# Optimization experiments

Hardware: AMD Instinct MI355X
Metric: run time of the kernel (lower is better)

The kernel has to match this reference:

```python
import jax, jax.numpy as jnp
import numpy as np

CODEBOOK_SIZE = 1024
CODEBOOK_DIM = 64
COMMITMENT_WEIGHT = 0.25
DECAY = 0.99
EPS = 1e-5


def setup_inputs() -> dict:
    key = jax.random.key(0)
    k1, k2, k3 = jax.random.split(key, 3)
    B, D, T = 32, CODEBOOK_DIM, 4096
    z = jax.random.normal(k1, (B, D, T), dtype=jnp.float32)
    embedding = jax.random.normal(k2, (CODEBOOK_SIZE, CODEBOOK_DIM), dtype=jnp.float32)
    cluster_size = jnp.zeros((CODEBOOK_SIZE,), dtype=jnp.float32)
    embed_avg = jax.random.normal(k3, (CODEBOOK_SIZE, CODEBOOK_DIM), dtype=jnp.float32)
    return {"z": z, "embedding": embedding, "cluster_size": cluster_size, "embed_avg": embed_avg}


def reference(z, embedding, cluster_size, embed_avg):
    # z: [B, D, T]; embedding/embed_avg: [K, D]; cluster_size: [K]
    B, D, T = z.shape
    K = embedding.shape[0]
    z_flat = jnp.transpose(z, (0, 2, 1)).reshape(-1, D)  # [N, D], N = B*T

    # squared-euclidean distances via expansion (matches torch cdist expansion)
    dist = (
        jnp.sum(z_flat * z_flat, axis=1, keepdims=True)
        + jnp.sum(embedding * embedding, axis=1)
        - 2.0 * (z_flat @ embedding.T)
    )  # [N, K]
    indices = jnp.argmin(dist, axis=1)  # [N] int

    # EMA updates (training path). one_hot.sum(0) -> segment count; one_hot.T @ z_flat -> segment sum
    counts = jax.ops.segment_sum(jnp.ones(z_flat.shape[0], dtype=z_flat.dtype), indices, num_segments=K)
    new_cluster_size = cluster_size * DECAY + (1.0 - DECAY) * counts
    embed_sum = jax.ops.segment_sum(z_flat, indices, num_segments=K)  # [K, D]
    new_embed_avg = embed_avg * DECAY + (1.0 - DECAY) * embed_sum
    n = jnp.sum(new_cluster_size)
    smoothed = (new_cluster_size + EPS) / (n + K * EPS) * n  # Laplace smoothing
    new_embedding = new_embed_avg / smoothed[:, None]  # [K, D]

    # quantize with the *updated* codebook (as in the torch in-place update)
    z_q_flat = new_embedding[indices]  # [N, D] gather
    loss = COMMITMENT_WEIGHT * jnp.mean((z_flat - jax.lax.stop_gradient(z_q_flat)) ** 2)
    # straight-through estimator
    z_q_flat = z_flat + jax.lax.stop_gradient(z_q_flat - z_flat)
    z_q = jnp.transpose(z_q_flat.reshape(B, T, D), (0, 2, 1))  # [B, D, T]
    return z_q, loss, indices.reshape(B, T)
```

## Files before the change

### kernel.cpp

```cpp
#include <hip/hip_runtime.h>

#define N_PTS 131072
#define TD 4096
#define DD 64
#define KK 1024
#define MARGIN_TH 2e-3f

typedef short bf16x8 __attribute__((ext_vector_type(8)));
typedef float f32x4  __attribute__((ext_vector_type(4)));

__device__ inline unsigned short f2bf(float f) {
    unsigned u = __float_as_uint(f);
    unsigned r = u + 0x7FFFu + ((u >> 16) & 1u);
    return (unsigned short)(r >> 16);
}
__device__ inline float bf2f(unsigned short h) {
    return __uint_as_float(((unsigned)h) << 16);
}

__global__ __launch_bounds__(256) void vq_prep(const float* __restrict__ z,
                                               unsigned short* __restrict__ zh,
                                               unsigned short* __restrict__ zl)
{
    __shared__ float tile[64][65];
    const int tid = threadIdx.x;
    const int b = blockIdx.x >> 6;
    const int t0 = (blockIdx.x & 63) * 64;

    const int d = tid >> 2, tq = tid & 3;
#pragma unroll
    for (int it = 0; it < 4; ++it) {
        const int tt = tq * 16 + it * 4;
        const float4 v = *(const float4*)(z + ((size_t)b * DD + d) * TD + t0 + tt);
        tile[d][tt] = v.x; tile[d][tt + 1] = v.y; tile[d][tt + 2] = v.z; tile[d][tt + 3] = v.w;
    }
    __syncthreads();

    const int p = tid >> 2, dg = tid & 3;
    bf16x8 h0, h1, l0, l1;
#pragma unroll
    for (int j = 0; j < 8; ++j) {
        const float v0 = -tile[dg * 16 + j][p];
        const unsigned short a = f2bf(v0);
        h0[j] = (short)a; l0[j] = (short)f2bf(v0 - bf2f(a));
        const float v1 = -tile[dg * 16 + 8 + j][p];
        const unsigned short c = f2bf(v1);
        h1[j] = (short)c; l1[j] = (short)f2bf(v1 - bf2f(c));
    }
    const size_t o = ((size_t)(b * TD + t0 + p)) * DD + dg * 16;
    *(bf16x8*)(zh + o) = h0;
    *(bf16x8*)(zh + o + 8) = h1;
    *(bf16x8*)(zl + o) = l0;
    *(bf16x8*)(zl + o + 8) = l1;
}

__global__ __launch_bounds__(256) void vq_eprep(const float* __restrict__ emb,
                                                unsigned short* __restrict__ efh,
                                                unsigned short* __restrict__ efl,
                                                float* __restrict__ halfnorm)
{
    const int k = blockIdx.x * 256 + threadIdx.x;
    if (k >= KK) return;
    const int t = k >> 4, col = k & 15;
    const float* e = emb + (size_t)k * DD;
    double s = 0.0;
#pragma unroll
    for (int d = 0; d < DD; ++d) {
        const float v = e[d];
        const double dv = (double)v;
        s = fma(dv, dv, s);
        const unsigned short h = f2bf(v);
        const int q = d >> 3, j = d & 7;
        const size_t pos = (size_t)t * 1024 + (q >> 2) * 512 + ((q & 3) * 16 + col) * 8 + j;
        efh[pos] = h;
        efl[pos] = f2bf(v - bf2f(h));
    }
    halfnorm[k] = (float)(0.5 * s);
}

__global__ __launch_bounds__(256, 4) void vq_screen_mfma(
    const unsigned short* __restrict__ zh, const unsigned short* __restrict__ zl,
    const unsigned short* __restrict__ efh, const unsigned short* __restrict__ efl,
    const float* __restrict__ hn,
    int* __restrict__ idx_ws, float* __restrict__ ind_out,
    int* __restrict__ nflag, int* __restrict__ flags, int* __restrict__ hist)
{
    const int tid  = threadIdx.x;
    const int lane = tid & 63;
    const int wv   = tid >> 6;
    const int quad = lane >> 4;
    const int col  = lane & 15;
    const int pbase = blockIdx.x * 128 + wv * 32;

    const bf16x8* pA0h = (const bf16x8*)(zh + (size_t)(pbase + col) * DD + quad * 8);
    const bf16x8* pA0l = (const bf16x8*)(zl + (size_t)(pbase + col) * DD + quad * 8);
    const bf16x8* pA1h = (const bf16x8*)(zh + (size_t)(pbase + 16 + col) * DD + quad * 8);
    const bf16x8* pA1l = (const bf16x8*)(zl + (size_t)(pbase + 16 + col) * DD + quad * 8);
    const bf16x8 A0h0 = pA0h[0], A0h1 = pA0h[4];
    const bf16x8 A0l0 = pA0l[0], A0l1 = pA0l[4];
    const bf16x8 A1h0 = pA1h[0], A1h1 = pA1h[4];
    const bf16x8 A1l0 = pA1l[0], A1l1 = pA1l[4];

    const unsigned short* fh = efh + lane * 8;
    const unsigned short* fl = efl + lane * 8;

    bf16x8 ch0 = *(const bf16x8*)(fh);
    bf16x8 ch1 = *(const bf16x8*)(fh + 512);
    bf16x8 cl0 = *(const bf16x8*)(fl);
    bf16x8 cl1 = *(const bf16x8*)(fl + 512);
    float chn = hn[col];

    float best0[4]  = {1e30f, 1e30f, 1e30f, 1e30f};
    float best20[4] = {1e30f, 1e30f, 1e30f, 1e30f};
    int   bidx0[4]  = {0, 0, 0, 0};
    float best1[4]  = {1e30f, 1e30f, 1e30f, 1e30f};
    float best21[4] = {1e30f, 1e30f, 1e30f, 1e30f};
    int   bidx1[4]  = {0, 0, 0, 0};

#pragma unroll 2
    for (int t = 0; t < KK / 16; ++t) {
        const int tn = (t + 1) & 63;
        const bf16x8 nh0 = *(const bf16x8*)(fh + tn * 1024);
        const bf16x8 nh1 = *(const bf16x8*)(fh + tn * 1024 + 512);
        const bf16x8 nl0 = *(const bf16x8*)(fl + tn * 1024);
        const bf16x8 nl1 = *(const bf16x8*)(fl + tn * 1024 + 512);
        const float  nhn = hn[tn * 16 + col];

        f32x4 a0 = {chn, chn, chn, chn};
        f32x4 a1 = {chn, chn, chn, chn};
        a0 = __builtin_amdgcn_mfma_f32_16x16x32_bf16(A0h0, ch0, a0, 0, 0, 0);
        a1 = __builtin_amdgcn_mfma_f32_16x16x32_bf16(A1h0, ch0, a1, 0, 0, 0);
        a0 = __builtin_amdgcn_mfma_f32_16x16x32_bf16(A0h1, ch1, a0, 0, 0, 0);
        a1 = __builtin_amdgcn_mfma_f32_16x16x32_bf16(A1h1, ch1, a1, 0, 0, 0);
        a0 = __builtin_amdgcn_mfma_f32_16x16x32_bf16(A0l0, ch0, a0, 0, 0, 0);
        a1 = __builtin_amdgcn_mfma_f32_16x16x32_bf16(A1l0, ch0, a1, 0, 0, 0);
        a0 = __builtin_amdgcn_mfma_f32_16x16x32_bf16(A0l1, ch1, a0, 0, 0, 0);
        a1 = __builtin_amdgcn_mfma_f32_16x16x32_bf16(A1l1, ch1, a1, 0, 0, 0);
        a0 = __builtin_amdgcn_mfma_f32_16x16x32_bf16(A0h0, cl0, a0, 0, 0, 0);
        a1 = __builtin_amdgcn_mfma_f32_16x16x32_bf16(A1h0, cl0, a1, 0, 0, 0);
        a0 = __builtin_amdgcn_mfma_f32_16x16x32_bf16(A0h1, cl1, a0, 0, 0, 0);
        a1 = __builtin_amdgcn_mfma_f32_16x16x32_bf16(A1h1, cl1, a1, 0, 0, 0);

        const int code = t * 16 + col;
#pragma unroll
        for (int r = 0; r < 4; ++r) {
            const float s0 = a0[r];
            best20[r] = __builtin_amdgcn_fmed3f(best0[r], best20[r], s0);
            if (s0 < best0[r]) { best0[r] = s0; bidx0[r] = code; }
            const float s1 = a1[r];
            best21[r] = __builtin_amdgcn_fmed3f(best1[r], best21[r], s1);
            if (s1 < best1[r]) { best1[r] = s1; bidx1[r] = code; }
        }

        ch0 = nh0; ch1 = nh1; cl0 = nl0; cl1 = nl1; chn = nhn;
    }

#pragma unroll
    for (int off = 1; off < 16; off <<= 1) {
#pragma unroll
        for (int r = 0; r < 4; ++r) {
            {
                const float ob  = __shfl_xor(best0[r],  off, 64);
                const float ob2 = __shfl_xor(best20[r], off, 64);
                const int   oi  = __shfl_xor(bidx0[r],  off, 64);
                const float nb2 = fminf(fminf(best20[r], ob2), fmaxf(best0[r], ob));
                if (ob < best0[r]) { best0[r] = ob; bidx0[r] = oi; }
                best20[r] = nb2;
            }
            {
                const float ob  = __shfl_xor(best1[r],  off, 64);
                const float ob2 = __shfl_xor(best21[r], off, 64);
                const int   oi  = __shfl_xor(bidx1[r],  off, 64);
                const float nb2 = fminf(fminf(best21[r], ob2), fmaxf(best1[r], ob));
                if (ob < best1[r]) { best1[r] = ob; bidx1[r] = oi; }
                best21[r] = nb2;
            }
        }
    }

    if (col == 0) {
#pragma unroll
        for (int r = 0; r < 4; ++r) {
            const int n0 = pbase + quad * 4 + r;
            idx_ws[n0] = bidx0[r];
            ind_out[n0] = (float)bidx0[r];
            atomicAdd(&hist[bidx0[r]], 1);
            if (best20[r] - best0[r] < MARGIN_TH) {
                const int pos = atomicAdd(nflag, 1);
                flags[pos] = n0;
            }
            const int n1 = pbase + 16 + quad * 4 + r;
            idx_ws[n1] = bidx1[r];
            ind_out[n1] = (float)bidx1[r];
            atomicAdd(&hist[bidx1[r]], 1);
            if (best21[r] - best1[r] < MARGIN_TH) {
                const int pos = atomicAdd(nflag, 1);
                flags[pos] = n1;
            }
        }
    }
}

__global__ __launch_bounds__(256) void vq_fallback(
    const float* __restrict__ z, const float* __restrict__ emb,
    int* __restrict__ idx_ws, float* __restrict__ ind_out,
    const int* __restrict__ nflag, const int* __restrict__ flags,
    int* __restrict__ hist)
{
    __shared__ float zs[4][DD];
    const int total = *nflag;
    const int lane = threadIdx.x & 63;
    const int wid = threadIdx.x >> 6;
    const int gw = blockIdx.x * 4 + wid;

    for (int i = gw; i < total; i += gridDim.x * 4) {
        const int n = flags[i];
        const int b = n >> 12, t = n & 4095;
        zs[wid][lane] = z[((size_t)b * DD + lane) * TD + t];
        __builtin_amdgcn_s_waitcnt(0);
        double best = 1e300;
        int bi = KK;
        for (int kc = 0; kc < KK / 64; ++kc) {
            const int k = kc * 64 + lane;
            const float4* e = (const float4*)(emb + (size_t)k * DD);
            double dot = 0.0, nn = 0.0;
#pragma unroll
            for (int j = 0; j < 16; ++j) {
                float4 ev = e[j];
                double e0 = (double)ev.x, e1 = (double)ev.y, e2 = (double)ev.z, e3 = (double)ev.w;
                nn = fma(e0, e0, fma(e1, e1, fma(e2, e2, fma(e3, e3, nn))));
                dot = fma((double)zs[wid][4 * j + 0], e0,
                      fma((double)zs[wid][4 * j + 1], e1,
                      fma((double)zs[wid][4 * j + 2], e2,
                      fma((double)zs[wid][4 * j + 3], e3, dot))));
            }
            double s = 0.5 * nn - dot;
            if (s < best || (s == best && k < bi)) { best = s; bi = k; }
        }
        for (int off = 32; off > 0; off >>= 1) {
            double os = __shfl_down(best, off, 64);
            int oi = __shfl_down(bi, off, 64);
            if (os < best || (os == best && oi < bi)) { best = os; bi = oi; }
        }
        if (lane == 0) {
            const int old = idx_ws[n];
            if (bi != old) {
                idx_ws[n] = bi;
                ind_out[n] = (float)bi;
                atomicAdd(&hist[old], -1);
                atomicAdd(&hist[bi], 1);
            }
        }
    }
}

__global__ __launch_bounds__(1024) void vq_prefix_smo(
    const int* __restrict__ hist, const float* __restrict__ cs,
    int* __restrict__ cursor, float* __restrict__ rsmo)
{
    __shared__ int tmp[KK];
    __shared__ double dred[KK];
    const int k = threadIdx.x;
    const int c = hist[k];
    tmp[k] = c;
    const double ncs = 0.99 * (double)cs[k] + 0.01 * (double)c;
    dred[k] = ncs;
    __syncthreads();
    for (int off = 1; off < KK; off <<= 1) {
        int u = (k >= off) ? tmp[k - off] : 0;
        __syncthreads();
        tmp[k] += u;
        __syncthreads();
    }
    cursor[k] = tmp[k] - c;
    for (int s = 512; s > 0; s >>= 1) {
        if (k < s) dred[k] += dred[k + s];
        __syncthreads();
    }
    const double nsum = dred[0];
    const double smo = (ncs + 1e-5) / (nsum + (double)KK * 1e-5) * nsum;
    rsmo[k] = (float)(1.0 / smo);
}

__global__ __launch_bounds__(256) void vq_scatter(const int* __restrict__ idx_ws,
                                                  int* __restrict__ cursor, int* __restrict__ order)
{
    const int n = blockIdx.x * 256 + threadIdx.x;
    const int bi = idx_ws[n];
    const int pos = atomicAdd(&cursor[bi], 1);
    order[pos] = n;
}

__global__ __launch_bounds__(256) void vq_esum2(
    const unsigned short* __restrict__ zh, const unsigned short* __restrict__ zl,
    const int* __restrict__ idx_ws, const int* __restrict__ order,
    float* __restrict__ esum)
{
    const int tid = threadIdx.x;
    const int lane = tid & 63;
    const int w = tid >> 6;
    const int base = blockIdx.x * 256 + w * 64;

    const int pid_l = order[base + lane];
    const int code_l = idx_ws[pid_l];

    float v[64];
#pragma unroll
    for (int j = 0; j < 64; ++j) {
        const int pj = __shfl(pid_l, j, 64);
        const size_t o = (size_t)pj * DD + lane;
        v[j] = bf2f(zh[o]) + bf2f(zl[o]);
    }

    float racc = 0.f;
    int cur = __shfl(code_l, 0, 64);
#pragma unroll
    for (int j = 0; j < 64; ++j) {
        const int cj = __shfl(code_l, j, 64);
        if (cj != cur) {
            atomicAdd(&esum[(size_t)cur * DD + lane], -racc);
            racc = 0.f;
            cur = cj;
        }
        racc += v[j];
    }
    atomicAdd(&esum[(size_t)cur * DD + lane], -racc);
}

__global__ __launch_bounds__(256) void vq_newE(
    const float* __restrict__ avg, const float* __restrict__ esum,
    const float* __restrict__ rsmo, float* __restrict__ newE)
{
    const int j = blockIdx.x * 256 + threadIdx.x;
    newE[j] = (float)((0.99 * (double)avg[j] + 0.01 * (double)esum[j]) * (double)rsmo[j >> 6]);
}

__global__ __launch_bounds__(256) void vq_gather_loss(
    const float* __restrict__ z, const float* __restrict__ newE,
    const int* __restrict__ idx_ws, float* __restrict__ zq_out,
    double* __restrict__ loss_acc, int* __restrict__ done_cnt,
    float* __restrict__ loss_out)
{
    const int tid = threadIdx.x;
    const int n = blockIdx.x * 256 + tid;
    const int b = n >> 12;
    const int t = n & 4095;
    const float* zb = z + ((size_t)b * DD) * TD + t;
    float* ob = zq_out + ((size_t)b * DD) * TD + t;
    const int bi = idx_ws[n];
    const float* e = newE + (size_t)bi * DD;
    double acc = 0.0;
#pragma unroll
    for (int d = 0; d < DD; ++d) {
        float q = e[d];
        float zv = zb[(size_t)d * TD];
        ob[(size_t)d * TD] = q;
        float df = zv - q;
        acc = fma((double)df, (double)df, acc);
    }
    for (int off = 32; off > 0; off >>= 1) acc += __shfl_down(acc, off, 64);
    __shared__ double wsum[4];
    const int wid = tid >> 6, lane = tid & 63;
    if (lane == 0) wsum[wid] = acc;
    __syncthreads();
    if (tid == 0) {
        atomicAdd(loss_acc, wsum[0] + wsum[1] + wsum[2] + wsum[3]);
        __threadfence();
        const int prev = atomicAdd(done_cnt, 1);
        if (prev == gridDim.x - 1) {
            __threadfence();
            *loss_out = (float)(0.25 * (*loss_acc) / (double)(N_PTS * DD));
        }
    }
}

extern "C" void kernel_launch(void* const* d_in, const int* in_sizes, int n_in,
                              void* d_out, int out_size, void* d_ws, size_t ws_size,
                              hipStream_t stream) {
    const float* z    = (const float*)d_in[0];
    const float* emb  = (const float*)d_in[1];
    const float* cs   = (const float*)d_in[2];
    const float* avg  = (const float*)d_in[3];

    float* out      = (float*)d_out;
    float* zq_out   = out;
    float* loss_out = out + 8388608;
    float* ind_out  = out + 8388609;

    unsigned short* zh = (unsigned short*)d_out;
    unsigned short* zl = (unsigned short*)((char*)d_out + 16777216);

    char* ws = (char*)d_ws;
    int*            idx_ws   = (int*)ws;
    float*          newE     = (float*)(ws + 524288);
    float*          esum     = (float*)(ws + 786432);
    int*            hist     = (int*)(ws + 1048576);
    int*            nflag    = (int*)(ws + 1052672);
    int*            done_cnt = (int*)(ws + 1052676);
    double*         loss_acc = (double*)(ws + 1052680);
    float*          halfnorm = (float*)(ws + 1052688);
    int*            cursor   = (int*)(ws + 1056784);
    int*            flags    = (int*)(ws + 1060880);
    int*            order    = (int*)(ws + 1585168);
    unsigned short* efh      = (unsigned short*)(ws + 2109456);
    unsigned short* efl      = (unsigned short*)(ws + 2240528);
    float*          rsmo     = (float*)(ws + 2371600);

    hipMemsetAsync(ws + 786432, 0, 266256, stream);

    vq_prep<<<2048, 256, 0, stream>>>(z, zh, zl);
    vq_eprep<<<4, 256, 0, stream>>>(emb, efh, efl, halfnorm);
    vq_screen_mfma<<<1024, 256, 0, stream>>>(zh, zl, efh, efl, halfnorm,
                                             idx_ws, ind_out, nflag, flags, hist);
    vq_fallback<<<128, 256, 0, stream>>>(z, emb, idx_ws, ind_out, nflag, flags, hist);
    vq_prefix_smo<<<1, 1024, 0, stream>>>(hist, cs, cursor, rsmo);
    vq_scatter<<<N_PTS / 256, 256, 0, stream>>>(idx_ws, cursor, order);
    vq_esum2<<<N_PTS / 256, 256, 0, stream>>>(zh, zl, idx_ws, order, esum);
    vq_newE<<<256, 256, 0, stream>>>(avg, esum, rsmo, newE);
    vq_gather_loss<<<N_PTS / 256, 256, 0, stream>>>(z, newE, idx_ws, zq_out,
                                                    loss_acc, done_cnt, loss_out);
}
```

Measured before the change: 342.0 us.

## Stage codebook tiles through LDS with async global-to-LDS loads and triple buffering

```diff
diff --git a/kernel.cpp b/kernel.cpp
--- a/kernel.cpp
+++ b/kernel.cpp
@@ -16,6 +16,12 @@
 }
 __device__ inline float bf2f(unsigned short h) {
     return __uint_as_float(((unsigned)h) << 16);
+}
+
+__device__ inline void gload_lds16(const unsigned short* g, unsigned short* l) {
+    __builtin_amdgcn_global_load_lds(
+        (const __attribute__((address_space(1))) unsigned int*)g,
+        (__attribute__((address_space(3))) unsigned int*)l, 16, 0, 0);
 }
 
 __global__ __launch_bounds__(256) void vq_prep(const float* __restrict__ z,
@@ -85,11 +91,15 @@
     int* __restrict__ idx_ws, float* __restrict__ ind_out,
     int* __restrict__ nflag, int* __restrict__ flags, int* __restrict__ hist)
 {
+    __shared__ __align__(16) unsigned short tiles[4][2048];
+    __shared__ float hns[KK];
+
     const int tid  = threadIdx.x;
     const int lane = tid & 63;
     const int wv   = tid >> 6;
     const int quad = lane >> 4;
     const int col  = lane & 15;
+    const int loff = lane * 8;
     const int pbase = blockIdx.x * 128 + wv * 32;
 
     const bf16x8* pA0h = (const bf16x8*)(zh + (size_t)(pbase + col) * DD + quad * 8);
@@ -101,14 +111,18 @@
     const bf16x8 A1h0 = pA1h[0], A1h1 = pA1h[4];
     const bf16x8 A1l0 = pA1l[0], A1l1 = pA1l[4];
 
-    const unsigned short* fh = efh + lane * 8;
-    const unsigned short* fl = efl + lane * 8;
-
-    bf16x8 ch0 = *(const bf16x8*)(fh);
-    bf16x8 ch1 = *(const bf16x8*)(fh + 512);
-    bf16x8 cl0 = *(const bf16x8*)(fl);
-    bf16x8 cl1 = *(const bf16x8*)(fl + 512);
-    float chn = hn[col];
+    ((float4*)hns)[tid] = ((const float4*)hn)[tid];
+
+    const unsigned short* sgl = (wv < 2 ? efh : efl) + (tid & 127) * 8;
+
+    asm volatile("s_waitcnt vmcnt(0)" ::: "memory");
+    __builtin_amdgcn_sched_barrier(0);
+    __syncthreads();
+
+#define SCREEN_STAGE(T) gload_lds16(sgl + (size_t)(T) * 1024, &tiles[(T) & 3][tid * 8])
+
+    SCREEN_STAGE(0);
+    SCREEN_STAGE(1);
 
     float best0[4]  = {1e30f, 1e30f, 1e30f, 1e30f};
     float best20[4] = {1e30f, 1e30f, 1e30f, 1e30f};
@@ -117,43 +131,61 @@
     float best21[4] = {1e30f, 1e30f, 1e30f, 1e30f};
     int   bidx1[4]  = {0, 0, 0, 0};
 
-#pragma unroll 2
-    for (int t = 0; t < KK / 16; ++t) {
-        const int tn = (t + 1) & 63;
-        const bf16x8 nh0 = *(const bf16x8*)(fh + tn * 1024);
-        const bf16x8 nh1 = *(const bf16x8*)(fh + tn * 1024 + 512);
-        const bf16x8 nl0 = *(const bf16x8*)(fl + tn * 1024);
-        const bf16x8 nl1 = *(const bf16x8*)(fl + tn * 1024 + 512);
-        const float  nhn = hn[tn * 16 + col];
-
-        f32x4 a0 = {chn, chn, chn, chn};
-        f32x4 a1 = {chn, chn, chn, chn};
-        a0 = __builtin_amdgcn_mfma_f32_16x16x32_bf16(A0h0, ch0, a0, 0, 0, 0);
-        a1 = __builtin_amdgcn_mfma_f32_16x16x32_bf16(A1h0, ch0, a1, 0, 0, 0);
-        a0 = __builtin_amdgcn_mfma_f32_16x16x32_bf16(A0h1, ch1, a0, 0, 0, 0);
-        a1 = __builtin_amdgcn_mfma_f32_16x16x32_bf16(A1h1, ch1, a1, 0, 0, 0);
-        a0 = __builtin_amdgcn_mfma_f32_16x16x32_bf16(A0l0, ch0, a0, 0, 0, 0);
-        a1 = __builtin_amdgcn_mfma_f32_16x16x32_bf16(A1l0, ch0, a1, 0, 0, 0);
-        a0 = __builtin_amdgcn_mfma_f32_16x16x32_bf16(A0l1, ch1, a0, 0, 0, 0);
-        a1 = __builtin_amdgcn_mfma_f32_16x16x32_bf16(A1l1, ch1, a1, 0, 0, 0);
-        a0 = __builtin_amdgcn_mfma_f32_16x16x32_bf16(A0h0, cl0, a0, 0, 0, 0);
-        a1 = __builtin_amdgcn_mfma_f32_16x16x32_bf16(A1h0, cl0, a1, 0, 0, 0);
-        a0 = __builtin_amdgcn_mfma_f32_16x16x32_bf16(A0h1, cl1, a0, 0, 0, 0);
-        a1 = __builtin_amdgcn_mfma_f32_16x16x32_bf16(A1h1, cl1, a1, 0, 0, 0);
-
-        const int code = t * 16 + col;
-#pragma unroll
-        for (int r = 0; r < 4; ++r) {
-            const float s0 = a0[r];
-            best20[r] = __builtin_amdgcn_fmed3f(best0[r], best20[r], s0);
-            if (s0 < best0[r]) { best0[r] = s0; bidx0[r] = code; }
-            const float s1 = a1[r];
-            best21[r] = __builtin_amdgcn_fmed3f(best1[r], best21[r], s1);
-            if (s1 < best1[r]) { best1[r] = s1; bidx1[r] = code; }
-        }
-
-        ch0 = nh0; ch1 = nh1; cl0 = nl0; cl1 = nl1; chn = nhn;
-    }
+#define SCREEN_BODY(T)                                                              \
+    {                                                                               \
+        const unsigned short* buf = &tiles[(T) & 3][0];                             \
+        const bf16x8 Bh0 = *(const bf16x8*)(buf + loff);                            \
+        const bf16x8 Bh1 = *(const bf16x8*)(buf + 512 + loff);                      \
+        const bf16x8 Bl0 = *(const bf16x8*)(buf + 1024 + loff);                     \
+        const bf16x8 Bl1 = *(const bf16x8*)(buf + 1536 + loff);                     \
+        const float chn = hns[(T) * 16 + col];                                      \
+        f32x4 a0 = {chn, chn, chn, chn};                                            \
+        f32x4 a1 = {chn, chn, chn, chn};                                            \
+        a0 = __builtin_amdgcn_mfma_f32_16x16x32_bf16(A0h0, Bh0, a0, 0, 0, 0);       \
+        a1 = __builtin_amdgcn_mfma_f32_16x16x32_bf16(A1h0, Bh0, a1, 0, 0, 0);       \
+        a0 = __builtin_amdgcn_mfma_f32_16x16x32_bf16(A0h1, Bh1, a0, 0, 0, 0);       \
+        a1 = __builtin_amdgcn_mfma_f32_16x16x32_bf16(A1h1, Bh1, a1, 0, 0, 0);       \
+        a0 = __builtin_amdgcn_mfma_f32_16x16x32_bf16(A0l0, Bh0, a0, 0, 0, 0);       \
+        a1 = __builtin_amdgcn_mfma_f32_16x16x32_bf16(A1l0, Bh0, a1, 0, 0, 0);       \
+        a0 = __builtin_amdgcn_mfma_f32_16x16x32_bf16(A0l1, Bh1, a0, 0, 0, 0);       \
+        a1 = __builtin_amdgcn_mfma_f32_16x16x32_bf16(A1l1, Bh1, a1, 0, 0, 0);       \
+        a0 = __builtin_amdgcn_mfma_f32_16x16x32_bf16(A0h0, Bl0, a0, 0, 0, 0);       \
+        a1 = __builtin_amdgcn_mfma_f32_16x16x32_bf16(A1h0, Bl0, a1, 0, 0, 0);       \
+        a0 = __builtin_amdgcn_mfma_f32_16x16x32_bf16(A0h1, Bl1, a0, 0, 0, 0);       \
+        a1 = __builtin_amdgcn_mfma_f32_16x16x32_bf16(A1h1, Bl1, a1, 0, 0, 0);       \
+        const int code = (T) * 16 + col;                                            \
+        _Pragma("unroll")                                                           \
+        for (int r = 0; r < 4; ++r) {                                               \
+            const float s0 = a0[r];                                                 \
+            best20[r] = __builtin_amdgcn_fmed3f(best0[r], best20[r], s0);           \
+            if (s0 < best0[r]) { best0[r] = s0; bidx0[r] = code; }                  \
+            const float s1 = a1[r];                                                 \
+            best21[r] = __builtin_amdgcn_fmed3f(best1[r], best21[r], s1);           \
+            if (s1 < best1[r]) { best1[r] = s1; bidx1[r] = code; }                  \
+        }                                                                           \
+    }
+
+    for (int t = 0; t < 62; ++t) {
+        SCREEN_STAGE(t + 2);
+        asm volatile("s_waitcnt vmcnt(2)" ::: "memory");
+        __builtin_amdgcn_sched_barrier(0);
+        __builtin_amdgcn_s_barrier();
+        __builtin_amdgcn_sched_barrier(0);
+        SCREEN_BODY(t);
+    }
+    asm volatile("s_waitcnt vmcnt(1)" ::: "memory");
+    __builtin_amdgcn_sched_barrier(0);
+    __builtin_amdgcn_s_barrier();
+    __builtin_amdgcn_sched_barrier(0);
+    SCREEN_BODY(62);
+    asm volatile("s_waitcnt vmcnt(0)" ::: "memory");
+    __builtin_amdgcn_sched_barrier(0);
+    __builtin_amdgcn_s_barrier();
+    __builtin_amdgcn_sched_barrier(0);
+    SCREEN_BODY(63);
+
+#undef SCREEN_STAGE
+#undef SCREEN_BODY
 
 #pragma unroll
     for (int off = 1; off < 16; off <<= 1) {
```

After: 342.6 us. Within noise of the previous version (+0.2%).

## Stage codebook tiles in LDS via direct global-to-LDS loads in screen kernel

Applied to the files above, without the earlier changes.

```diff
diff --git a/kernel.cpp b/kernel.cpp
--- a/kernel.cpp
+++ b/kernel.cpp
@@ -16,6 +16,12 @@
 }
 __device__ inline float bf2f(unsigned short h) {
     return __uint_as_float(((unsigned)h) << 16);
+}
+
+__device__ inline void gload_lds16(const unsigned short* g, unsigned short* l) {
+    __builtin_amdgcn_global_load_lds(
+        (const __attribute__((address_space(1))) unsigned int*)g,
+        (__attribute__((address_space(3))) unsigned int*)l, 16, 0, 0);
 }
 
 __global__ __launch_bounds__(256) void vq_prep(const float* __restrict__ z,
@@ -78,19 +84,22 @@
     halfnorm[k] = (float)(0.5 * s);
 }
 
-__global__ __launch_bounds__(256, 4) void vq_screen_mfma(
+__global__ __launch_bounds__(512, 4) void vq_screen_mfma(
     const unsigned short* __restrict__ zh, const unsigned short* __restrict__ zl,
     const unsigned short* __restrict__ efh, const unsigned short* __restrict__ efl,
     const float* __restrict__ hn,
     int* __restrict__ idx_ws, float* __restrict__ ind_out,
     int* __restrict__ nflag, int* __restrict__ flags, int* __restrict__ hist)
 {
+    __shared__ __align__(16) unsigned short tiles[16][2048];
+
     const int tid  = threadIdx.x;
     const int lane = tid & 63;
     const int wv   = tid >> 6;
     const int quad = lane >> 4;
     const int col  = lane & 15;
-    const int pbase = blockIdx.x * 128 + wv * 32;
+    const int loff = lane * 8;
+    const int pbase = blockIdx.x * 256 + wv * 32;
 
     const bf16x8* pA0h = (const bf16x8*)(zh + (size_t)(pbase + col) * DD + quad * 8);
     const bf16x8* pA0l = (const bf16x8*)(zl + (size_t)(pbase + col) * DD + quad * 8);
@@ -101,15 +110,6 @@
     const bf16x8 A1h0 = pA1h[0], A1h1 = pA1h[4];
     const bf16x8 A1l0 = pA1l[0], A1l1 = pA1l[4];
 
-    const unsigned short* fh = efh + lane * 8;
-    const unsigned short* fl = efl + lane * 8;
-
-    bf16x8 ch0 = *(const bf16x8*)(fh);
-    bf16x8 ch1 = *(const bf16x8*)(fh + 512);
-    bf16x8 cl0 = *(const bf16x8*)(fl);
-    bf16x8 cl1 = *(const bf16x8*)(fl + 512);
-    float chn = hn[col];
-
     float best0[4]  = {1e30f, 1e30f, 1e30f, 1e30f};
     float best20[4] = {1e30f, 1e30f, 1e30f, 1e30f};
     int   bidx0[4]  = {0, 0, 0, 0};
@@ -117,42 +117,57 @@
     float best21[4] = {1e30f, 1e30f, 1e30f, 1e30f};
     int   bidx1[4]  = {0, 0, 0, 0};
 
+    for (int Q = 0; Q < 4; ++Q) {
+        __syncthreads();
+
+#pragma unroll
+        for (int k = 0; k < 8; ++k) {
+            const int T = Q * 16 + wv * 2 + (k >> 2);
+            const unsigned short* src =
+                ((k & 2) ? efl : efh) + (size_t)T * 1024 + (k & 1) * 512 + loff;
+            unsigned short* dst =
+                &tiles[0][0] + (wv * 2 + (k >> 2)) * 2048 + (k & 3) * 512 + loff;
+            gload_lds16(src, dst);
+        }
+        asm volatile("s_waitcnt vmcnt(0)" ::: "memory");
+        __syncthreads();
+
 #pragma unroll 2
-    for (int t = 0; t < KK / 16; ++t) {
-        const int tn = (t + 1) & 63;
-        const bf16x8 nh0 = *(const bf16x8*)(fh + tn * 1024);
-        const bf16x8 nh1 = *(const bf16x8*)(fh + tn * 1024 + 512);
-        const bf16x8 nl0 = *(const bf16x8*)(fl + tn * 1024);
-        const bf16x8 nl1 = *(const bf16x8*)(fl + tn * 1024 + 512);
-        const float  nhn = hn[tn * 16 + col];
-
-        f32x4 a0 = {chn, chn, chn, chn};
-        f32x4 a1 = {chn, chn, chn, chn};
-        a0 = __builtin_amdgcn_mfma_f32_16x16x32_bf16(A0h0, ch0, a0, 0, 0, 0);
-        a1 = __builtin_amdgcn_mfma_f32_16x16x32_bf16(A1h0, ch0, a1, 0, 0, 0);
-        a0 = __builtin_amdgcn_mfma_f32_16x16x32_bf16(A0h1, ch1, a0, 0, 0, 0);
-        a1 = __builtin_amdgcn_mfma_f32_16x16x32_bf16(A1h1, ch1, a1, 0, 0, 0);
-        a0 = __builtin_amdgcn_mfma_f32_16x16x32_bf16(A0l0, ch0, a0, 0, 0, 0);
-        a1 = __builtin_amdgcn_mfma_f32_16x16x32_bf16(A1l0, ch0, a1, 0, 0, 0);
-        a0 = __builtin_amdgcn_mfma_f32_16x16x32_bf16(A0l1, ch1, a0, 0, 0, 0);
-        a1 = __builtin_amdgcn_mfma_f32_16x16x32_bf16(A1l1, ch1, a1, 0, 0, 0);
-        a0 = __builtin_amdgcn_mfma_f32_16x16x32_bf16(A0h0, cl0, a0, 0, 0, 0);
-        a1 = __builtin_amdgcn_mfma_f32_16x16x32_bf16(A1h0, cl0, a1, 0, 0, 0);
-        a0 = __builtin_amdgcn_mfma_f32_16x16x32_bf16(A0h1, cl1, a0, 0, 0, 0);
-        a1 = __builtin_amdgcn_mfma_f32_16x16x32_bf16(A1h1, cl1, a1, 0, 0, 0);
-
-        const int code = t * 16 + col;
-#pragma unroll
-        for (int r = 0; r < 4; ++r) {
-            const float s0 = a0[r];
-            best20[r] = __builtin_amdgcn_fmed3f(best0[r], best20[r], s0);
-            if (s0 < best0[r]) { best0[r] = s0; bidx0[r] = code; }
-            const float s1 = a1[r];
-            best21[r] = __builtin_amdgcn_fmed3f(best1[r], best21[r], s1);
-            if (s1 < best1[r]) { best1[r] = s1; bidx1[r] = code; }
-        }
-
-        ch0 = nh0; ch1 = nh1; cl0 = nl0; cl1 = nl1; chn = nhn;
+        for (int tt = 0; tt < 16; ++tt) {
+            const unsigned short* buf = &tiles[tt][0];
+            const bf16x8 Bh0 = *(const bf16x8*)(buf + loff);
+            const bf16x8 Bh1 = *(const bf16x8*)(buf + 512 + loff);
+            const bf16x8 Bl0 = *(const bf16x8*)(buf + 1024 + loff);
+            const bf16x8 Bl1 = *(const bf16x8*)(buf + 1536 + loff);
+            const int tg = Q * 16 + tt;
+            const float chn = hn[tg * 16 + col];
+
+            f32x4 p0 = {chn, chn, chn, chn}, q0 = {0.f, 0.f, 0.f, 0.f};
+            f32x4 p1 = {chn, chn, chn, chn}, q1 = {0.f, 0.f, 0.f, 0.f};
+            p0 = __builtin_amdgcn_mfma_f32_16x16x32_bf16(A0h0, Bh0, p0, 0, 0, 0);
+            p1 = __builtin_amdgcn_mfma_f32_16x16x32_bf16(A1h0, Bh0, p1, 0, 0, 0);
+            q0 = __builtin_amdgcn_mfma_f32_16x16x32_bf16(A0l0, Bh0, q0, 0, 0, 0);
+            q1 = __builtin_amdgcn_mfma_f32_16x16x32_bf16(A1l0, Bh0, q1, 0, 0, 0);
+            p0 = __builtin_amdgcn_mfma_f32_16x16x32_bf16(A0h1, Bh1, p0, 0, 0, 0);
+            p1 = __builtin_amdgcn_mfma_f32_16x16x32_bf16(A1h1, Bh1, p1, 0, 0, 0);
+            q0 = __builtin_amdgcn_mfma_f32_16x16x32_bf16(A0l1, Bh1, q0, 0, 0, 0);
+            q1 = __builtin_amdgcn_mfma_f32_16x16x32_bf16(A1l1, Bh1, q1, 0, 0, 0);
+            p0 = __builtin_amdgcn_mfma_f32_16x16x32_bf16(A0h0, Bl0, p0, 0, 0, 0);
+            p1 = __builtin_amdgcn_mfma_f32_16x16x32_bf16(A1h0, Bl0, p1, 0, 0, 0);
+            p0 = __builtin_amdgcn_mfma_f32_16x16x32_bf16(A0h1, Bl1, p0, 0, 0, 0);
+            p1 = __builtin_amdgcn_mfma_f32_16x16x32_bf16(A1h1, Bl1, p1, 0, 0, 0);
+
+            const int code = tg * 16 + col;
+#pragma unroll
+            for (int r = 0; r < 4; ++r) {
+                const float s0 = p0[r] + q0[r];
+                best20[r] = __builtin_amdgcn_fmed3f(best0[r], best20[r], s0);
+                if (s0 < best0[r]) { best0[r] = s0; bidx0[r] = code; }
+                const float s1 = p1[r] + q1[r];
+                best21[r] = __builtin_amdgcn_fmed3f(best1[r], best21[r], s1);
+                if (s1 < best1[r]) { best1[r] = s1; bidx1[r] = code; }
+            }
+        }
     }
 
 #pragma unroll
@@ -410,8 +425,8 @@
 
     vq_prep<<<2048, 256, 0, stream>>>(z, zh, zl);
     vq_eprep<<<4, 256, 0, stream>>>(emb, efh, efl, halfnorm);
-    vq_screen_mfma<<<1024, 256, 0, stream>>>(zh, zl, efh, efl, halfnorm,
-                                             idx_ws, ind_out, nflag, flags, hist);
+    vq_screen_mfma<<<512, 512, 0, stream>>>(zh, zl, efh, efl, halfnorm,
+                                            idx_ws, ind_out, nflag, flags, hist);
     vq_fallback<<<128, 256, 0, stream>>>(z, emb, idx_ws, ind_out, nflag, flags, hist);
     vq_prefix_smo<<<1, 1024, 0, stream>>>(hist, cs, cursor, rsmo);
     vq_scatter<<<N_PTS / 256, 256, 0, stream>>>(idx_ws, cursor, order);
```

Result: faster. 334.3 us (-2.3%).

## Stage codebook tiles in LDS with double buffering and move histogram to separate kernel

Applied to the files above, without the earlier changes.

```diff
diff --git a/kernel.cpp b/kernel.cpp
--- a/kernel.cpp
+++ b/kernel.cpp
@@ -78,103 +78,88 @@
     halfnorm[k] = (float)(0.5 * s);
 }
 
-__global__ __launch_bounds__(256, 4) void vq_screen_mfma(
+__global__ __launch_bounds__(256, 6) void vq_screen_mfma(
     const unsigned short* __restrict__ zh, const unsigned short* __restrict__ zl,
     const unsigned short* __restrict__ efh, const unsigned short* __restrict__ efl,
     const float* __restrict__ hn,
     int* __restrict__ idx_ws, float* __restrict__ ind_out,
-    int* __restrict__ nflag, int* __restrict__ flags, int* __restrict__ hist)
-{
+    int* __restrict__ nflag, int* __restrict__ flags)
+{
+    __shared__ __align__(16) unsigned short tiles[2][2048];
+
     const int tid  = threadIdx.x;
     const int lane = tid & 63;
     const int wv   = tid >> 6;
     const int quad = lane >> 4;
     const int col  = lane & 15;
-    const int pbase = blockIdx.x * 128 + wv * 32;
-
-    const bf16x8* pA0h = (const bf16x8*)(zh + (size_t)(pbase + col) * DD + quad * 8);
-    const bf16x8* pA0l = (const bf16x8*)(zl + (size_t)(pbase + col) * DD + quad * 8);
-    const bf16x8* pA1h = (const bf16x8*)(zh + (size_t)(pbase + 16 + col) * DD + quad * 8);
-    const bf16x8* pA1l = (const bf16x8*)(zl + (size_t)(pbase + 16 + col) * DD + quad * 8);
-    const bf16x8 A0h0 = pA0h[0], A0h1 = pA0h[4];
-    const bf16x8 A0l0 = pA0l[0], A0l1 = pA0l[4];
-    const bf16x8 A1h0 = pA1h[0], A1h1 = pA1h[4];
-    const bf16x8 A1l0 = pA1l[0], A1l1 = pA1l[4];
-
-    const unsigned short* fh = efh + lane * 8;
-    const unsigned short* fl = efl + lane * 8;
-
-    bf16x8 ch0 = *(const bf16x8*)(fh);
-    bf16x8 ch1 = *(const bf16x8*)(fh + 512);
-    bf16x8 cl0 = *(const bf16x8*)(fl);
-    bf16x8 cl1 = *(const bf16x8*)(fl + 512);
+    const int loff = lane * 8;
+    const int pbase = blockIdx.x * 64 + wv * 16;
+
+    const bf16x8* ph = (const bf16x8*)(zh + (size_t)(pbase + col) * DD + quad * 8);
+    const bf16x8* pl = (const bf16x8*)(zl + (size_t)(pbase + col) * DD + quad * 8);
+    const bf16x8 Ah0 = ph[0], Ah1 = ph[4];
+    const bf16x8 Al0 = pl[0], Al1 = pl[4];
+
+    const unsigned short* sg = (tid < 128) ? (efh + tid * 8) : (efl + (tid - 128) * 8);
+
+    *(bf16x8*)(&tiles[0][tid * 8]) = *(const bf16x8*)(sg);
     float chn = hn[col];
 
-    float best0[4]  = {1e30f, 1e30f, 1e30f, 1e30f};
-    float best20[4] = {1e30f, 1e30f, 1e30f, 1e30f};
-    int   bidx0[4]  = {0, 0, 0, 0};
-    float best1[4]  = {1e30f, 1e30f, 1e30f, 1e30f};
-    float best21[4] = {1e30f, 1e30f, 1e30f, 1e30f};
-    int   bidx1[4]  = {0, 0, 0, 0};
-
-#pragma unroll 2
+    float best[4]  = {1e30f, 1e30f, 1e30f, 1e30f};
+    float best2[4] = {1e30f, 1e30f, 1e30f, 1e30f};
+    int   bidx[4]  = {0, 0, 0, 0};
+
+    __syncthreads();
+
     for (int t = 0; t < KK / 16; ++t) {
-        const int tn = (t + 1) & 63;
-        const bf16x8 nh0 = *(const bf16x8*)(fh + tn * 1024);
-        const bf16x8 nh1 = *(const bf16x8*)(fh + tn * 1024 + 512);
-        const bf16x8 nl0 = *(const bf16x8*)(fl + tn * 1024);
-        const bf16x8 nl1 = *(const bf16x8*)(fl + tn * 1024 + 512);
-        const float  nhn = hn[tn * 16 + col];
-
-        f32x4 a0 = {chn, chn, chn, chn};
-        f32x4 a1 = {chn, chn, chn, chn};
-        a0 = __builtin_amdgcn_mfma_f32_16x16x32_bf16(A0h0, ch0, a0, 0, 0, 0);
-        a1 = __builtin_amdgcn_mfma_f32_16x16x32_bf16(A1h0, ch0, a1, 0, 0, 0);
-        a0 = __builtin_amdgcn_mfma_f32_16x16x32_bf16(A0h1, ch1, a0, 0, 0, 0);
-        a1 = __builtin_amdgcn_mfma_f32_16x16x32_bf16(A1h1, ch1, a1, 0, 0, 0);
-        a0 = __builtin_amdgcn_mfma_f32_16x16x32_bf16(A0l0, ch0, a0, 0, 0, 0);
-        a1 = __builtin_amdgcn_mfma_f32_16x16x32_bf16(A1l0, ch0, a1, 0, 0, 0);
-        a0 = __builtin_amdgcn_mfma_f32_16x16x32_bf16(A0l1, ch1, a0, 0, 0, 0);
-        a1 = __builtin_amdgcn_mfma_f32_16x16x32_bf16(A1l1, ch1, a1, 0, 0, 0);
-        a0 = __builtin_amdgcn_mfma_f32_16x16x32_bf16(A0h0, cl0, a0, 0, 0, 0);
-        a1 = __builtin_amdgcn_mfma_f32_16x16x32_bf16(A1h0, cl0, a1, 0, 0, 0);
-        a0 = __builtin_amdgcn_mfma_f32_16x16x32_bf16(A0h1, cl1, a0, 0, 0, 0);
-        a1 = __builtin_amdgcn_mfma_f32_16x16x32_bf16(A1h1, cl1, a1, 0, 0, 0);
+        const int cur = t & 1;
+
+        bf16x8 nr;
+        float nhn = 0.f;
+        if (t < 63) {
+            nr = *(const bf16x8*)(sg + (size_t)(t + 1) * 1024);
+            nhn = hn[(t + 1) * 16 + col];
+        }
+
+        const unsigned short* buf = &tiles[cur][0];
+        const bf16x8 Bh0 = *(const bf16x8*)(buf + loff);
+        const bf16x8 Bh1 = *(const bf16x8*)(buf + 512 + loff);
+        const bf16x8 Bl0 = *(const bf16x8*)(buf + 1024 + loff);
+        const bf16x8 Bl1 = *(const bf16x8*)(buf + 1536 + loff);
+
+        if (t < 63) *(bf16x8*)(&tiles[cur ^ 1][tid * 8]) = nr;
+
+        f32x4 p = {chn, chn, chn, chn};
+        p = __builtin_amdgcn_mfma_f32_16x16x32_bf16(Ah0, Bh0, p, 0, 0, 0);
+        p = __builtin_amdgcn_mfma_f32_16x16x32_bf16(Ah1, Bh1, p, 0, 0, 0);
+        p = __builtin_amdgcn_mfma_f32_16x16x32_bf16(Al0, Bh0, p, 0, 0, 0);
+        p = __builtin_amdgcn_mfma_f32_16x16x32_bf16(Al1, Bh1, p, 0, 0, 0);
+        p = __builtin_amdgcn_mfma_f32_16x16x32_bf16(Ah0, Bl0, p, 0, 0, 0);
+        p = __builtin_amdgcn_mfma_f32_16x16x32_bf16(Ah1, Bl1, p, 0, 0, 0);
 
         const int code = t * 16 + col;
 #pragma unroll
         for (int r = 0; r < 4; ++r) {
-            const float s0 = a0[r];
-            best20[r] = __builtin_amdgcn_fmed3f(best0[r], best20[r], s0);
-            if (s0 < best0[r]) { best0[r] = s0; bidx0[r] = code; }
-            const float s1 = a1[r];
-            best21[r] = __builtin_amdgcn_fmed3f(best1[r], best21[r], s1);
-            if (s1 < best1[r]) { best1[r] = s1; bidx1[r] = code; }
-        }
-
-        ch0 = nh0; ch1 = nh1; cl0 = nl0; cl1 = nl1; chn = nhn;
+            const float s = p[r];
+            best2[r] = __builtin_amdgcn_fmed3f(best[r], best2[r], s);
+            bidx[r] = (s < best[r]) ? code : bidx[r];
+            best[r] = fminf(best[r], s);
+        }
+
+        __syncthreads();
+        chn = nhn;
     }
 
 #pragma unroll
     for (int off = 1; off < 16; off <<= 1) {
 #pragma unroll
         for (int r = 0; r < 4; ++r) {
-            {
-                const float ob  = __shfl_xor(best0[r],  off, 64);
-                const float ob2 = __shfl_xor(best20[r], off, 64);
-                const int   oi  = __shfl_xor(bidx0[r],  off, 64);
-                const float nb2 = fminf(fminf(best20[r], ob2), fmaxf(best0[r], ob));
-                if (ob < best0[r]) { best0[r] = ob; bidx0[r] = oi; }
-                best20[r] = nb2;
-            }
-            {
-                const float ob  = __shfl_xor(best1[r],  off, 64);
-                const float ob2 = __shfl_xor(best21[r], off, 64);
-                const int   oi  = __shfl_xor(bidx1[r],  off, 64);
-                const float nb2 = fminf(fminf(best21[r], ob2), fmaxf(best1[r], ob));
-                if (ob < best1[r]) { best1[r] = ob; bidx1[r] = oi; }
-                best21[r] = nb2;
-            }
+            const float ob  = __shfl_xor(best[r],  off, 64);
+            const float ob2 = __shfl_xor(best2[r], off, 64);
+            const int   oi  = __shfl_xor(bidx[r],  off, 64);
+            const float nb2 = fminf(fminf(best2[r], ob2), fmaxf(best[r], ob));
+            if (ob < best[r]) { best[r] = ob; bidx[r] = oi; }
+            best2[r] = nb2;
         }
     }
 
@@ -182,21 +167,12 @@
 #pragma unroll
         for (int r = 0; r < 4; ++r) {
             const int n0 = pbase + quad * 4 + r;
-            idx_ws[n0] = bidx0[r];
-            ind_out[n0] = (float)bidx0[r];
-            atomicAdd(&hist[bidx0[r]], 1);
-            if (best20[r] - best0[r] < MARGIN_TH) {
+            idx_ws[n0] = bidx[r];
+            ind_out[n0] = (float)bidx[r];
+            if (best2[r] - best[r] < MARGIN_TH) {
                 const int pos = atomicAdd(nflag, 1);
                 flags[pos] = n0;
             }
-            const int n1 = pbase + 16 + quad * 4 + r;
-            idx_ws[n1] = bidx1[r];
-            ind_out[n1] = (float)bidx1[r];
-            atomicAdd(&hist[bidx1[r]], 1);
-            if (best21[r] - best1[r] < MARGIN_TH) {
-                const int pos = atomicAdd(nflag, 1);
-                flags[pos] = n1;
-            }
         }
     }
 }
@@ -204,8 +180,7 @@
 __global__ __launch_bounds__(256) void vq_fallback(
     const float* __restrict__ z, const float* __restrict__ emb,
     int* __restrict__ idx_ws, float* __restrict__ ind_out,
-    const int* __restrict__ nflag, const int* __restrict__ flags,
-    int* __restrict__ hist)
+    const int* __restrict__ nflag, const int* __restrict__ flags)
 {
     __shared__ float zs[4][DD];
     const int total = *nflag;
@@ -242,16 +217,22 @@
             int oi = __shfl_down(bi, off, 64);
             if (os < best || (os == best && oi < bi)) { best = os; bi = oi; }
         }
-        if (lane == 0) {
-            const int old = idx_ws[n];
-            if (bi != old) {
-                idx_ws[n] = bi;
-                ind_out[n] = (float)bi;
-                atomicAdd(&hist[old], -1);
-                atomicAdd(&hist[bi], 1);
-            }
-        }
-    }
+        if (lane == 0) { idx_ws[n] = bi; ind_out[n] = (float)bi; }
+    }
+}
+
+__global__ __launch_bounds__(256) void vq_hist(const int* __restrict__ idx_ws, int* __restrict__ hist)
+{
+    __shared__ int h[KK];
+    for (int i = threadIdx.x; i < KK; i += 256) h[i] = 0;
+    __syncthreads();
+    const int base = blockIdx.x * 2048;
+#pragma unroll
+    for (int j = 0; j < 8; ++j)
+        atomicAdd(&h[idx_ws[base + j * 256 + threadIdx.x]], 1);
+    __syncthreads();
+    for (int i = threadIdx.x; i < KK; i += 256)
+        if (h[i]) atomicAdd(&hist[i], h[i]);
 }
 
 __global__ __launch_bounds__(1024) void vq_prefix_smo(
@@ -410,9 +391,10 @@
 
     vq_prep<<<2048, 256, 0, stream>>>(z, zh, zl);
     vq_eprep<<<4, 256, 0, stream>>>(emb, efh, efl, halfnorm);
-    vq_screen_mfma<<<1024, 256, 0, stream>>>(zh, zl, efh, efl, halfnorm,
-                                             idx_ws, ind_out, nflag, flags, hist);
-    vq_fallback<<<128, 256, 0, stream>>>(z, emb, idx_ws, ind_out, nflag, flags, hist);
+    vq_screen_mfma<<<N_PTS / 64, 256, 0, stream>>>(zh, zl, efh, efl, halfnorm,
+                                                   idx_ws, ind_out, nflag, flags);
+    vq_fallback<<<128, 256, 0, stream>>>(z, emb, idx_ws, ind_out, nflag, flags);
+    vq_hist<<<64, 256, 0, stream>>>(idx_ws, hist);
     vq_prefix_smo<<<1, 1024, 0, stream>>>(hist, cs, cursor, rsmo);
     vq_scatter<<<N_PTS / 256, 256, 0, stream>>>(idx_ws, cursor, order);
     vq_esum2<<<N_PTS / 256, 256, 0, stream>>>(zh, zl, idx_ws, order, esum);
```

Result: faster. 294.4 us (-13.9%).
